# Optimization experiments

Hardware: AMD Instinct MI355X
Metric: run time of the kernel (lower is better)

Reference implementation:

```python
import jax, jax.numpy as jnp
import numpy as np

B = 32768
Z_DIM = 64
X_DIM = 256
HIDDEN = 512
T = 8            # num_transforms
NBINS = 8
TAIL = 25.0
MULT = 3 * NBINS - 1   # widths + heights + interior derivatives = 23
MIN_W = 1e-3
MIN_H = 1e-3
MIN_D = 1e-3


def _masks():
    # MADE degrees (nflows, random_mask=False)
    d_in = np.arange(1, Z_DIM + 1)                      # input degrees 1..D
    h = np.arange(HIDDEN) % (Z_DIM - 1) + 1             # hidden degrees
    o = np.arange(Z_DIM * MULT) // MULT + 1             # output degrees, MULT contiguous per feature
    m1 = (h[:, None] >= d_in[None, :]).astype(np.float32)   # [H, D]
    m2 = (h[:, None] >= h[None, :]).astype(np.float32)      # [H, H]
    m3 = (o[:, None] > h[None, :]).astype(np.float32)       # [D*MULT, H] strict for output layer
    return jnp.asarray(m1), jnp.asarray(m2), jnp.asarray(m3)


def _rq_spline_fwd(z, uw, uh, ud):
    """Unconstrained rational-quadratic spline with linear tails (forward).
    z: [B, D]; uw/uh: [B, D, NBINS]; ud: [B, D, NBINS-1].
    Returns (outputs [B,D], logabsdet [B,D])."""
    const = np.log(np.exp(1.0 - MIN_D) - 1.0)
    pad = jnp.full(ud.shape[:-1] + (1,), const, ud.dtype)
    ud = jnp.concatenate([pad, ud, pad], axis=-1)       # [B, D, NBINS+1]

    widths = jax.nn.softmax(uw, axis=-1)
    widths = MIN_W + (1.0 - MIN_W * NBINS) * widths
    zero = jnp.zeros(widths.shape[:-1] + (1,), widths.dtype)
    cumw = jnp.concatenate([zero, jnp.cumsum(widths, axis=-1)], axis=-1)
    cumw = -TAIL + 2.0 * TAIL * cumw
    cumw = cumw.at[..., 0].set(-TAIL).at[..., -1].set(TAIL)
    widths = cumw[..., 1:] - cumw[..., :-1]

    derivs = MIN_D + jax.nn.softplus(ud)

    heights = jax.nn.softmax(uh, axis=-1)
    heights = MIN_H + (1.0 - MIN_H * NBINS) * heights
    cumh = jnp.concatenate([zero, jnp.cumsum(heights, axis=-1)], axis=-1)
    cumh = -TAIL + 2.0 * TAIL * cumh
    cumh = cumh.at[..., 0].set(-TAIL).at[..., -1].set(TAIL)
    heights = cumh[..., 1:] - cumh[..., :-1]

    delta = heights / widths

    z_in = jnp.clip(z, -TAIL, TAIL)
    edges = cumw.at[..., -1].add(1e-6)                  # nflows searchsorted eps
    idx = jnp.sum(z_in[..., None] >= edges, axis=-1) - 1
    idx = jnp.clip(idx, 0, NBINS - 1)

    g = lambda a: jnp.take_along_axis(a, idx[..., None], axis=-1)[..., 0]
    in_cw = g(cumw); in_w = g(widths)
    in_ch = g(cumh); in_h = g(heights)
    in_dl = g(delta)
    d0 = g(derivs); d1 = g(derivs[..., 1:])

    th = (z_in - in_cw) / in_w
    th1 = th * (1.0 - th)
    num = in_h * (in_dl * th * th + d0 * th1)
    den = in_dl + (d0 + d1 - 2.0 * in_dl) * th1
    out = in_ch + num / den
    dnum = in_dl ** 2 * (d1 * th * th + 2.0 * in_dl * th1 + d0 * (1.0 - th) ** 2)
    lad = jnp.log(dnum) - 2.0 * jnp.log(den)

    inside = (z >= -TAIL) & (z <= TAIL)
    return jnp.where(inside, out, z), jnp.where(inside, lad, 0.0)


def setup_inputs() -> dict:
    key = jax.random.key(0)
    ks = jax.random.split(key, 10)
    s = 0.05  # small init scale keeps spline params in a sane regime
    return {
        "z": jax.random.normal(ks[0], (B, Z_DIM), jnp.float32),
        "x": jax.random.normal(ks[1], (B, X_DIM), jnp.float32),
        "W1": jax.random.normal(ks[2], (T, HIDDEN, Z_DIM), jnp.float32) * s,
        "b1": jax.random.normal(ks[3], (T, HIDDEN), jnp.float32) * s,
        "Wc": jax.random.normal(ks[4], (T, HIDDEN, X_DIM), jnp.float32) * s,
        "bc": jax.random.normal(ks[5], (T, HIDDEN), jnp.float32) * s,
        "W2": jax.random.normal(ks[6], (T, HIDDEN, HIDDEN), jnp.float32) * s,
        "b2": jax.random.normal(ks[7], (T, HIDDEN), jnp.float32) * s,
        "W3": jax.random.normal(ks[8], (T, Z_DIM * MULT, HIDDEN), jnp.float32) * s,
        "b3": jax.random.normal(ks[9], (T, Z_DIM * MULT), jnp.float32) * s,
    }


def reference(z, x, W1, b1, Wc, bc, W2, b2, W3, b3):
    """log q(z|x) of the composed MADE-RQ-spline flow, shape [B]."""
    m1, m2, m3 = _masks()
    inv_sqrt_h = 1.0 / np.sqrt(HIDDEN)
    cur = z
    total_lad = jnp.zeros(z.shape[0], z.dtype)
    for t in range(T):
        # MADE: masked initial layer + context layer, one masked feedforward block (linear->relu), masked output layer
        h = cur @ (W1[t] * m1).T + b1[t] + x @ Wc[t].T + bc[t]
        h = jax.nn.relu(h @ (W2[t] * m2).T + b2[t])
        p = (h @ (W3[t] * m3).T + b3[t]).reshape(-1, Z_DIM, MULT)
        uw = p[..., :NBINS] * inv_sqrt_h
        uh = p[..., NBINS:2 * NBINS] * inv_sqrt_h
        ud = p[..., 2 * NBINS:]
        cur, lad = _rq_spline_fwd(cur, uw, uh, ud)
        total_lad = total_lad + lad.sum(axis=-1)
    log_base = -0.5 * jnp.sum(cur ** 2, axis=-1) - 0.5 * Z_DIM * np.log(2.0 * np.pi)
    return log_base + total_lad
```

## Files before the change

### kernel.cpp

```cpp
#include <hip/hip_runtime.h>
#include <cstdint>
#include <cstddef>

#define B_ROWS 32768
#define ZD 64
#define XD 256
#define HID 512
#define T_STEPS 8
#define MULT 23
#define MPAD 24
#define NOUT 1472
#define NPAD 1536
#define K1 320
#define PSTRIDE 200

typedef float f32x4 __attribute__((ext_vector_type(4)));
typedef short s16x8 __attribute__((ext_vector_type(8)));

__device__ __forceinline__ unsigned short f2bf(float f) {
  unsigned int u = __float_as_uint(f);
  u = (u + 0x7FFFu + ((u >> 16) & 1u)) >> 16;
  return (unsigned short)u;
}
__device__ __forceinline__ float bf2f(unsigned short s) {
  return __uint_as_float(((unsigned int)s) << 16);
}

__device__ __forceinline__ int permP(int n) {
  return (n < 72) ? (n / 9) + 63 * (n % 9)
                  : ((n - 72) >> 3) + 8 + 63 * ((n - 72) & 7);
}
__device__ __forceinline__ int degP(int n) {
  return (n < 72) ? (n / 9) + 1 : ((n - 72) >> 3) + 9;
}


__global__ void prep_w1cat(const float* __restrict__ W1, const float* __restrict__ Wc,
                           unsigned short* __restrict__ o) {
  int i = blockIdx.x * 256 + threadIdx.x;
  if (i >= T_STEPS * HID * K1) return;
  int t = i / (HID * K1);
  int r = i - t * (HID * K1);
  int n = r / K1;
  int k = r - n * K1;
  int on = permP(n);
  float v;
  if (k < ZD) {
    v = ((on % 63) >= k) ? W1[((size_t)t * HID + on) * ZD + k] : 0.0f;
  } else {
    v = Wc[((size_t)t * HID + on) * XD + (k - ZD)];
  }
  o[i] = f2bf(v);
}

__global__ void prep_w2(const float* __restrict__ W2, unsigned short* __restrict__ o) {
  int i = blockIdx.x * 256 + threadIdx.x;
  if (i >= T_STEPS * HID * HID) return;
  int t = i / (HID * HID);
  int r = i - t * (HID * HID);
  int n = r / HID;
  int k = r - n * HID;
  float v = 0.0f;
  if (degP(n) >= degP(k))
    v = W2[((size_t)t * HID + permP(n)) * HID + permP(k)];
  o[i] = f2bf(v);
}

__global__ void prep_w3(const float* __restrict__ W3, unsigned short* __restrict__ o) {
  int i = blockIdx.x * 256 + threadIdx.x;
  if (i >= T_STEPS * NPAD * HID) return;
  int t = i / (NPAD * HID);
  int r = i - t * (NPAD * HID);
  int n = r / HID;
  int k = r - n * HID;
  int d = n / MPAD;
  int jj = n - d * MPAD;
  float v = 0.0f;
  if (jj < MULT && d >= degP(k))
    v = W3[((size_t)t * NOUT + d * MULT + jj) * HID + permP(k)];
  o[i] = f2bf(v);
}

__global__ void prep_bias(const float* __restrict__ b1, const float* __restrict__ bc,
                          const float* __restrict__ b2, const float* __restrict__ b3,
                          float* __restrict__ ob1, float* __restrict__ ob2,
                          float* __restrict__ ob3) {
  int i = blockIdx.x * 256 + threadIdx.x;
  if (i < T_STEPS * HID) {
    int t = i / HID, n = i - t * HID;
    int on = permP(n);
    ob1[i] = b1[(size_t)t * HID + on] + bc[(size_t)t * HID + on];
  } else if (i < 2 * T_STEPS * HID) {
    int j = i - T_STEPS * HID;
    int t = j / HID, n = j - t * HID;
    ob2[j] = b2[(size_t)t * HID + permP(n)];
  } else {
    int j = i - 2 * T_STEPS * HID;
    if (j < T_STEPS * NPAD) {
      int t = j / NPAD;
      int n = j - t * NPAD;
      int d = n / MPAD;
      int jj = n - d * MPAD;
      ob3[j] = (jj < MULT) ? b3[(size_t)t * NOUT + d * MULT + jj] : 0.0f;
    }
  }
}

__global__ void prep_x(const float* __restrict__ x, unsigned short* __restrict__ A1) {
  int i = blockIdx.x * 256 + threadIdx.x;
  if (i >= B_ROWS * XD) return;
  int b = i >> 8;
  int j = i & 255;
  A1[(size_t)b * K1 + ZD + j] = f2bf(x[i]);
}

__global__ void prep_init(const float* __restrict__ z, unsigned short* __restrict__ A1,
                          float* __restrict__ curf, float* __restrict__ lad) {
  int i = blockIdx.x * 256 + threadIdx.x;
  if (i >= B_ROWS * ZD) return;
  int b = i >> 6;
  int d = i & 63;
  float zv = z[i];
  A1[(size_t)b * K1 + d] = f2bf(zv);
  curf[i] = zv;
  if (d == 0) lad[b] = 0.0f;
}


#define ASYNC16(gp, lp) __builtin_amdgcn_global_load_lds( \
    (__attribute__((address_space(1))) unsigned int*)(gp), \
    (__attribute__((address_space(3))) unsigned int*)(lp), 16, 0, 0)


__global__ __launch_bounds__(256, 2) void gemm_bias(
    const unsigned short* __restrict__ A,
    const unsigned short* __restrict__ Bw,
    const float* __restrict__ bias,
    unsigned short* __restrict__ C,
    int M, int N, int K, int relu, int tri)
{
  __shared__ alignas(16) unsigned short lA[2 * 128 * 32];
  __shared__ alignas(16) unsigned short lB[2 * 128 * 32];

  const int tid  = threadIdx.x;
  const int lane = tid & 63;
  const int wave = tid >> 6;

  const int lin = blockIdx.y * 4 + blockIdx.x;
  const int xcd = lin & 7;
  const int loc = lin >> 3;
  const int m0 = (xcd * 32 + (loc >> 2)) * 128;
  const int n0 = (loc & 3) * 128;
  const int Keff = tri ? min(K, 192 + n0) : K;

  const int wm = (wave >> 1) * 64;
  const int wn = (wave & 1) * 64;

  const int f    = tid * 16;
  const int row0 = f >> 6;
  const int colb = f & 63;

  char* gA0 = (char*)A  + ((size_t)(m0 + row0) * K) * 2 + colb;
  char* gA1 = gA0 + (size_t)64 * K * 2;
  char* gB0 = (char*)Bw + ((size_t)(n0 + row0) * K) * 2 + colb;
  char* gB1 = gB0 + (size_t)64 * K * 2;

  unsigned short* lA0 = lA + wave * 512;
  unsigned short* lA1 = lA + 2048 + wave * 512;
  unsigned short* lB0 = lB + wave * 512;
  unsigned short* lB1 = lB + 2048 + wave * 512;

  f32x4 acc[4][4];
#pragma unroll
  for (int i = 0; i < 4; i++)
#pragma unroll
    for (int j = 0; j < 4; j++) acc[i][j] = (f32x4){0.f, 0.f, 0.f, 0.f};

  const int fr = lane & 15;
  const int fk = (lane >> 4) * 8;

  for (int k0 = 0; k0 < Keff; k0 += 64) {
    ASYNC16(gA0, lA0);
    ASYNC16(gA1, lA1);
    ASYNC16(gB0, lB0);
    ASYNC16(gB1, lB1);
    ASYNC16(gA0 + 64, lA0 + 4096);
    ASYNC16(gA1 + 64, lA1 + 4096);
    ASYNC16(gB0 + 64, lB0 + 4096);
    ASYNC16(gB1 + 64, lB1 + 4096);
    gA0 += 128; gA1 += 128; gB0 += 128; gB1 += 128;
    __syncthreads();

    s16x8 a0[4], b0[4], a1[4], b1[4];
#pragma unroll
    for (int i = 0; i < 4; i++) {
      a0[i] = *(const s16x8*)(lA + (wm + i * 16 + fr) * 32 + fk);
      a1[i] = *(const s16x8*)(lA + 4096 + (wm + i * 16 + fr) * 32 + fk);
    }
#pragma unroll
    for (int j = 0; j < 4; j++) {
      b0[j] = *(const s16x8*)(lB + (wn + j * 16 + fr) * 32 + fk);
      b1[j] = *(const s16x8*)(lB + 4096 + (wn + j * 16 + fr) * 32 + fk);
    }

#pragma unroll
    for (int i = 0; i < 4; i++)
#pragma unroll
      for (int j = 0; j < 4; j++)
        acc[i][j] = __builtin_amdgcn_mfma_f32_16x16x32_bf16(a0[i], b0[j], acc[i][j], 0, 0, 0);
#pragma unroll
    for (int i = 0; i < 4; i++)
#pragma unroll
      for (int j = 0; j < 4; j++)
        acc[i][j] = __builtin_amdgcn_mfma_f32_16x16x32_bf16(a1[i], b1[j], acc[i][j], 0, 0, 0);
    __syncthreads();
  }

#pragma unroll
  for (int j = 0; j < 4; j++) {
    const int col = n0 + wn + j * 16 + fr;
    const float bv = bias[col];
#pragma unroll
    for (int i = 0; i < 4; i++) {
      const int rbase = m0 + wm + i * 16 + (lane >> 4) * 4;
#pragma unroll
      for (int r = 0; r < 4; r++) {
        float v = acc[i][j][r] + bv;
        if (relu) v = fmaxf(v, 0.0f);
        C[(size_t)(rbase + r) * N + col] = f2bf(v);
      }
    }
  }
}


__device__ __forceinline__ void rq_spline(const unsigned short* __restrict__ pp,
                                          float zv, float& zn, float& lad) {
  const float TAILC = 25.0f;
  const float MIN_WC = 0.001f;
  const float MIN_DC = 0.001f;
  const float SCALE = 0.044194173824159216f;

  s16x8 vw = *(const s16x8*)(pp);
  s16x8 vh = *(const s16x8*)(pp + 8);
  s16x8 vd = *(const s16x8*)(pp + 16);

  bool inside = (zv >= -TAILC) && (zv <= TAILC);
  float z_in = fminf(fmaxf(zv, -TAILC), TAILC);

  float ew[8], eh[8], sw = 0.f, sh = 0.f;
#pragma unroll
  for (int i = 0; i < 8; i++) {
    float u = fminf(fmaxf(bf2f((unsigned short)vw[i]) * SCALE, -30.f), 30.f);
    ew[i] = __expf(u); sw += ew[i];
  }
#pragma unroll
  for (int i = 0; i < 8; i++) {
    float u = fminf(fmaxf(bf2f((unsigned short)vh[i]) * SCALE, -30.f), 30.f);
    eh[i] = __expf(u); sh += eh[i];
  }
  float iw = (1.0f - 8.0f * MIN_WC) / sw;
  float ih = (1.0f - 8.0f * MIN_WC) / sh;

  float cumw[9], cumh[9];
  cumw[0] = -TAILC; cumh[0] = -TAILC;
  float cw = 0.f, ch = 0.f;
#pragma unroll
  for (int i = 0; i < 8; i++) {
    cw += MIN_WC + ew[i] * iw;
    ch += MIN_WC + eh[i] * ih;
    cumw[i + 1] = fmaf(2.0f * TAILC, cw, -TAILC);
    cumh[i + 1] = fmaf(2.0f * TAILC, ch, -TAILC);
  }
  cumw[8] = TAILC; cumh[8] = TAILC;

  int idx = 0;
#pragma unroll
  for (int i = 1; i < 8; i++) idx += (z_in >= cumw[i]) ? 1 : 0;

  float in_cw = 0.f, cw1 = 1.f, in_ch = 0.f, ch1 = 1.f, u0 = 0.f, u1 = 0.f;
#pragma unroll
  for (int i = 0; i < 8; i++) {
    if (i == idx) {
      in_cw = cumw[i]; cw1 = cumw[i + 1];
      in_ch = cumh[i]; ch1 = cumh[i + 1];
      u0 = (i > 0) ? bf2f((unsigned short)vd[i - 1]) : 0.0f;
      u1 = (i < 7) ? bf2f((unsigned short)vd[i]) : 0.0f;
    }
  }
  float dd0 = (idx == 0) ? 1.0f
            : MIN_DC + fmaxf(u0, 0.f) + __logf(1.0f + __expf(-fabsf(u0)));
  float dd1 = (idx == 7) ? 1.0f
            : MIN_DC + fmaxf(u1, 0.f) + __logf(1.0f + __expf(-fabsf(u1)));
  float in_w = cw1 - in_cw;
  float in_h = ch1 - in_ch;

  float delta = in_h / in_w;
  float th  = (z_in - in_cw) / in_w;
  float th1 = th * (1.0f - th);
  float th2 = th * th;
  float num = in_h * (delta * th2 + dd0 * th1);
  float den = delta + (dd0 + dd1 - 2.0f * delta) * th1;
  float outz = in_ch + num / den;
  float omt = 1.0f - th;
  float dnum = delta * delta * (dd1 * th2 + 2.0f * delta * th1 + dd0 * omt * omt);
  float l = __logf(dnum) - 2.0f * __logf(den);

  zn  = inside ? outz : zv;
  lad = inside ? l : 0.0f;
}


__global__ __launch_bounds__(256, 2) void gemm3_spline(
    const unsigned short* __restrict__ A,
    const unsigned short* __restrict__ Bw,
    const float* __restrict__ bias,
    float* __restrict__ curf,
    unsigned short* __restrict__ A1,
    float* __restrict__ lad_acc)
{
  __shared__ alignas(16) union {
    struct { unsigned short A[2 * 128 * 32]; unsigned short B[2 * 192 * 32]; } g;
    unsigned short p[128 * PSTRIDE];
  } sm;

  const int tid  = threadIdx.x;
  const int lane = tid & 63;
  const int wave = tid >> 6;

  const int lin = blockIdx.y * 8 + blockIdx.x;
  const int xcd = lin & 7;
  const int loc = lin >> 3;
  const int m0 = (xcd * 32 + (loc >> 3)) * 128;
  const int bn = loc & 7;
  const int n0 = bn * 192;
  const int Keff = 64 * (bn + 1);

  const int wm = (wave >> 1) * 64;
  const int wn = (wave & 1) * 96;
  const int fr = lane & 15;
  const int fk = (lane >> 4) * 8;

  const int srow = tid & 127;
  const int sb = m0 + srow;
  const int dl0 = (tid >> 7) * 4;
  const int d0 = bn * 8 + dl0;
  float4 cz = *(const float4*)(curf + (size_t)sb * ZD + d0);
  float bv[6];
#pragma unroll
  for (int j = 0; j < 6; j++) bv[j] = bias[n0 + wn + j * 16 + fr];

  const int f    = tid * 16;
  const int row0 = f >> 6;
  const int colb = f & 63;
  const int K = HID;

  char* gA0 = (char*)A  + ((size_t)(m0 + row0) * K) * 2 + colb;
  char* gA1 = gA0 + (size_t)64 * K * 2;
  char* gB0 = (char*)Bw + ((size_t)(n0 + row0) * K) * 2 + colb;
  char* gB1 = gB0 + (size_t)64 * K * 2;
  char* gB2 = gB1 + (size_t)64 * K * 2;

  unsigned short* lA0 = sm.g.A + wave * 512;
  unsigned short* lA1 = sm.g.A + 2048 + wave * 512;
  unsigned short* lB0 = sm.g.B + wave * 512;
  unsigned short* lB1 = sm.g.B + 2048 + wave * 512;
  unsigned short* lB2 = sm.g.B + 4096 + wave * 512;

  f32x4 acc[4][6];
#pragma unroll
  for (int i = 0; i < 4; i++)
#pragma unroll
    for (int j = 0; j < 6; j++) acc[i][j] = (f32x4){0.f, 0.f, 0.f, 0.f};

  for (int k0 = 0; k0 < Keff; k0 += 64) {
    ASYNC16(gA0, lA0);
    ASYNC16(gA1, lA1);
    ASYNC16(gB0, lB0);
    ASYNC16(gB1, lB1);
    ASYNC16(gB2, lB2);
    ASYNC16(gA0 + 64, lA0 + 4096);
    ASYNC16(gA1 + 64, lA1 + 4096);
    ASYNC16(gB0 + 64, lB0 + 6144);
    ASYNC16(gB1 + 64, lB1 + 6144);
    ASYNC16(gB2 + 64, lB2 + 6144);
    gA0 += 128; gA1 += 128; gB0 += 128; gB1 += 128; gB2 += 128;
    __syncthreads();

    s16x8 a0[4], a1[4], b0[6], b1[6];
#pragma unroll
    for (int i = 0; i < 4; i++) {
      a0[i] = *(const s16x8*)(sm.g.A + (wm + i * 16 + fr) * 32 + fk);
      a1[i] = *(const s16x8*)(sm.g.A + 4096 + (wm + i * 16 + fr) * 32 + fk);
    }
#pragma unroll
    for (int j = 0; j < 6; j++) {
      b0[j] = *(const s16x8*)(sm.g.B + (wn + j * 16 + fr) * 32 + fk);
      b1[j] = *(const s16x8*)(sm.g.B + 6144 + (wn + j * 16 + fr) * 32 + fk);
    }

#pragma unroll
    for (int i = 0; i < 4; i++)
#pragma unroll
      for (int j = 0; j < 6; j++)
        acc[i][j] = __builtin_amdgcn_mfma_f32_16x16x32_bf16(a0[i], b0[j], acc[i][j], 0, 0, 0);
#pragma unroll
    for (int i = 0; i < 4; i++)
#pragma unroll
      for (int j = 0; j < 6; j++)
        acc[i][j] = __builtin_amdgcn_mfma_f32_16x16x32_bf16(a1[i], b1[j], acc[i][j], 0, 0, 0);
    __syncthreads();
  }

#pragma unroll
  for (int j = 0; j < 6; j++) {
    const int col = wn + j * 16 + fr;
#pragma unroll
    for (int i = 0; i < 4; i++) {
      const int rbase = wm + i * 16 + (lane >> 4) * 4;
#pragma unroll
      for (int r = 0; r < 4; r++)
        sm.p[(rbase + r) * PSTRIDE + col] = f2bf(acc[i][j][r] + bv[j]);
    }
  }
  __syncthreads();

  const unsigned short* pp = sm.p + srow * PSTRIDE + dl0 * MPAD;
  float zn0, zn1, zn2, zn3, l0, l1, l2, l3;
  rq_spline(pp,            cz.x, zn0, l0);
  rq_spline(pp + MPAD,     cz.y, zn1, l1);
  rq_spline(pp + 2 * MPAD, cz.z, zn2, l2);
  rq_spline(pp + 3 * MPAD, cz.w, zn3, l3);

  *(float4*)(curf + (size_t)sb * ZD + d0) = make_float4(zn0, zn1, zn2, zn3);
  union { unsigned int u[2]; unsigned short s[4]; } pk;
  pk.s[0] = f2bf(zn0); pk.s[1] = f2bf(zn1); pk.s[2] = f2bf(zn2); pk.s[3] = f2bf(zn3);
  *(uint2*)(A1 + (size_t)sb * K1 + d0) = make_uint2(pk.u[0], pk.u[1]);

  atomicAdd(&lad_acc[sb], l0 + l1 + l2 + l3);
}


__global__ void finalize(const float* __restrict__ curf, const float* __restrict__ lad,
                         float* __restrict__ out) {
  int i = blockIdx.x * 256 + threadIdx.x;
  int b = i >> 6;
  int d = i & 63;
  float c = curf[i];
  float q = c * c;
#pragma unroll
  for (int off = 32; off > 0; off >>= 1) q += __shfl_xor(q, off, 64);
  if (d == 0) out[b] = lad[b] - 0.5f * q - 58.81206612509905f;
}


extern "C" void kernel_launch(void* const* d_in, const int* in_sizes, int n_in,
                              void* d_out, int out_size, void* d_ws, size_t ws_size,
                              hipStream_t stream)
{
  const float* z  = (const float*)d_in[0];
  const float* x  = (const float*)d_in[1];
  const float* W1 = (const float*)d_in[2];
  const float* b1 = (const float*)d_in[3];
  const float* Wc = (const float*)d_in[4];
  const float* bc = (const float*)d_in[5];
  const float* W2 = (const float*)d_in[6];
  const float* b2 = (const float*)d_in[7];
  const float* W3 = (const float*)d_in[8];
  const float* b3 = (const float*)d_in[9];
  float* out = (float*)d_out;
  char* ws = (char*)d_ws;

  size_t oA1 = 0;
  size_t oH1 = oA1 + (size_t)B_ROWS * K1 * 2;
  size_t oH2 = oH1 + (size_t)B_ROWS * HID * 2;
  size_t oCU = oH2 + (size_t)B_ROWS * HID * 2;
  size_t oLA = oCU + (size_t)B_ROWS * ZD * 4;
  size_t oW1 = oLA + (size_t)B_ROWS * 4;
  size_t oW2 = oW1 + (size_t)T_STEPS * HID * K1 * 2;
  size_t oW3 = oW2 + (size_t)T_STEPS * HID * HID * 2;
  size_t oB1 = oW3 + (size_t)T_STEPS * NPAD * HID * 2;
  size_t oB2 = oB1 + (size_t)T_STEPS * HID * 4;
  size_t oB3 = oB2 + (size_t)T_STEPS * HID * 4;

  unsigned short* A1  = (unsigned short*)(ws + oA1);
  unsigned short* h1  = (unsigned short*)(ws + oH1);
  unsigned short* h2  = (unsigned short*)(ws + oH2);
  float* curf = (float*)(ws + oCU);
  float* lad  = (float*)(ws + oLA);
  unsigned short* w1c = (unsigned short*)(ws + oW1);
  unsigned short* w2c = (unsigned short*)(ws + oW2);
  unsigned short* w3c = (unsigned short*)(ws + oW3);
  float* b1c = (float*)(ws + oB1);
  float* b2p = (float*)(ws + oB2);
  float* b3c = (float*)(ws + oB3);

  prep_w1cat<<<T_STEPS * HID * K1 / 256, 256, 0, stream>>>(W1, Wc, w1c);
  prep_w2<<<T_STEPS * HID * HID / 256, 256, 0, stream>>>(W2, w2c);
  prep_w3<<<T_STEPS * NPAD * HID / 256, 256, 0, stream>>>(W3, w3c);
  prep_bias<<<T_STEPS * (2 * HID + NPAD) / 256, 256, 0, stream>>>(
      b1, bc, b2, b3, b1c, b2p, b3c);
  prep_x<<<B_ROWS * XD / 256, 256, 0, stream>>>(x, A1);
  prep_init<<<B_ROWS * ZD / 256, 256, 0, stream>>>(z, A1, curf, lad);

  for (int t = 0; t < T_STEPS; ++t) {
    gemm_bias<<<dim3(4, B_ROWS / 128), 256, 0, stream>>>(
        A1, w1c + (size_t)t * HID * K1, b1c + (size_t)t * HID, h1,
        B_ROWS, HID, K1, 0, 0);
    gemm_bias<<<dim3(4, B_ROWS / 128), 256, 0, stream>>>(
        h1, w2c + (size_t)t * HID * HID, b2p + (size_t)t * HID, h2,
        B_ROWS, HID, HID, 1, 1);
    gemm3_spline<<<dim3(8, B_ROWS / 128), 256, 0, stream>>>(
        h2, w3c + (size_t)t * NPAD * HID, b3c + (size_t)t * NPAD,
        curf, A1, lad);
  }
  finalize<<<B_ROWS * ZD / 256, 256, 0, stream>>>(curf, lad, out);
}
```

Before: 989.2 us.

## Merge prep kernels, fold finalize into last spline step, use exp2/log2

Merges the six preprocessing kernels into two launches and removes the finalize kernel. The last spline step now adds the base log-density term directly into the output through atomics, and the output is initialised with the constant. The spline math uses exp2f/log2 with pre-scaled constants and drops the clamps, and the GEMM launch bounds are raised to 3 blocks per SM. This trims launch count and a pass over curf, but may add register pressure, and removing the clamps risks overflow for large logits.

New measurement: 963.3 us. 1.03x faster.

```diff
diff --git a/kernel.cpp b/kernel.cpp
--- a/kernel.cpp
+++ b/kernel.cpp
@@ -35,95 +35,92 @@
 }
 
 
-__global__ void prep_w1cat(const float* __restrict__ W1, const float* __restrict__ Wc,
-                           unsigned short* __restrict__ o) {
+__global__ void prep_weights(const float* __restrict__ W1, const float* __restrict__ Wc,
+                             const float* __restrict__ W2, const float* __restrict__ W3,
+                             const float* __restrict__ b1, const float* __restrict__ bc,
+                             const float* __restrict__ b2, const float* __restrict__ b3,
+                             unsigned short* __restrict__ w1c, unsigned short* __restrict__ w2c,
+                             unsigned short* __restrict__ w3c,
+                             float* __restrict__ ob1, float* __restrict__ ob2,
+                             float* __restrict__ ob3) {
+  const int S1 = T_STEPS * HID * K1;
+  const int S2 = S1 + T_STEPS * HID * HID;
+  const int S3 = S2 + T_STEPS * NPAD * HID;
+  const int S4 = S3 + T_STEPS * HID;
+  const int S5 = S4 + T_STEPS * HID;
+  const int S6 = S5 + T_STEPS * NPAD;
   int i = blockIdx.x * 256 + threadIdx.x;
-  if (i >= T_STEPS * HID * K1) return;
-  int t = i / (HID * K1);
-  int r = i - t * (HID * K1);
-  int n = r / K1;
-  int k = r - n * K1;
-  int on = permP(n);
-  float v;
-  if (k < ZD) {
-    v = ((on % 63) >= k) ? W1[((size_t)t * HID + on) * ZD + k] : 0.0f;
-  } else {
-    v = Wc[((size_t)t * HID + on) * XD + (k - ZD)];
-  }
-  o[i] = f2bf(v);
-}
-
-__global__ void prep_w2(const float* __restrict__ W2, unsigned short* __restrict__ o) {
-  int i = blockIdx.x * 256 + threadIdx.x;
-  if (i >= T_STEPS * HID * HID) return;
-  int t = i / (HID * HID);
-  int r = i - t * (HID * HID);
-  int n = r / HID;
-  int k = r - n * HID;
-  float v = 0.0f;
-  if (degP(n) >= degP(k))
-    v = W2[((size_t)t * HID + permP(n)) * HID + permP(k)];
-  o[i] = f2bf(v);
-}
-
-__global__ void prep_w3(const float* __restrict__ W3, unsigned short* __restrict__ o) {
-  int i = blockIdx.x * 256 + threadIdx.x;
-  if (i >= T_STEPS * NPAD * HID) return;
-  int t = i / (NPAD * HID);
-  int r = i - t * (NPAD * HID);
-  int n = r / HID;
-  int k = r - n * HID;
-  int d = n / MPAD;
-  int jj = n - d * MPAD;
-  float v = 0.0f;
-  if (jj < MULT && d >= degP(k))
-    v = W3[((size_t)t * NOUT + d * MULT + jj) * HID + permP(k)];
-  o[i] = f2bf(v);
-}
-
-__global__ void prep_bias(const float* __restrict__ b1, const float* __restrict__ bc,
-                          const float* __restrict__ b2, const float* __restrict__ b3,
-                          float* __restrict__ ob1, float* __restrict__ ob2,
-                          float* __restrict__ ob3) {
-  int i = blockIdx.x * 256 + threadIdx.x;
-  if (i < T_STEPS * HID) {
-    int t = i / HID, n = i - t * HID;
+  if (i < S1) {
+    int t = i / (HID * K1);
+    int r = i - t * (HID * K1);
+    int n = r / K1;
+    int k = r - n * K1;
     int on = permP(n);
-    ob1[i] = b1[(size_t)t * HID + on] + bc[(size_t)t * HID + on];
-  } else if (i < 2 * T_STEPS * HID) {
-    int j = i - T_STEPS * HID;
+    float v;
+    if (k < ZD) v = ((on % 63) >= k) ? W1[((size_t)t * HID + on) * ZD + k] : 0.0f;
+    else        v = Wc[((size_t)t * HID + on) * XD + (k - ZD)];
+    w1c[i] = f2bf(v);
+  } else if (i < S2) {
+    int j = i - S1;
+    int t = j / (HID * HID);
+    int r = j - t * (HID * HID);
+    int n = r / HID;
+    int k = r - n * HID;
+    float v = 0.0f;
+    if (degP(n) >= degP(k))
+      v = W2[((size_t)t * HID + permP(n)) * HID + permP(k)];
+    w2c[j] = f2bf(v);
+  } else if (i < S3) {
+    int j = i - S2;
+    int t = j / (NPAD * HID);
+    int r = j - t * (NPAD * HID);
+    int n = r / HID;
+    int k = r - n * HID;
+    int d = n / MPAD;
+    int jj = n - d * MPAD;
+    float v = 0.0f;
+    if (jj < MULT && d >= degP(k))
+      v = W3[((size_t)t * NOUT + d * MULT + jj) * HID + permP(k)];
+    w3c[j] = f2bf(v);
+  } else if (i < S4) {
+    int j = i - S3;
+    int t = j / HID, n = j - t * HID;
+    int on = permP(n);
+    ob1[j] = b1[(size_t)t * HID + on] + bc[(size_t)t * HID + on];
+  } else if (i < S5) {
+    int j = i - S4;
     int t = j / HID, n = j - t * HID;
     ob2[j] = b2[(size_t)t * HID + permP(n)];
+  } else if (i < S6) {
+    int j = i - S5;
+    int t = j / NPAD;
+    int n = j - t * NPAD;
+    int d = n / MPAD;
+    int jj = n - d * MPAD;
+    ob3[j] = (jj < MULT) ? b3[(size_t)t * NOUT + d * MULT + jj] : 0.0f;
+  }
+}
+
+__global__ void prep_data(const float* __restrict__ x, const float* __restrict__ z,
+                          unsigned short* __restrict__ A1,
+                          float* __restrict__ curf, float* __restrict__ out) {
+  const int SX = B_ROWS * XD;
+  int i = blockIdx.x * 256 + threadIdx.x;
+  if (i < SX) {
+    int b = i >> 8;
+    int j = i & 255;
+    A1[(size_t)b * K1 + ZD + j] = f2bf(x[i]);
   } else {
-    int j = i - 2 * T_STEPS * HID;
-    if (j < T_STEPS * NPAD) {
-      int t = j / NPAD;
-      int n = j - t * NPAD;
-      int d = n / MPAD;
-      int jj = n - d * MPAD;
-      ob3[j] = (jj < MULT) ? b3[(size_t)t * NOUT + d * MULT + jj] : 0.0f;
-    }
-  }
-}
-
-__global__ void prep_x(const float* __restrict__ x, unsigned short* __restrict__ A1) {
-  int i = blockIdx.x * 256 + threadIdx.x;
-  if (i >= B_ROWS * XD) return;
-  int b = i >> 8;
-  int j = i & 255;
-  A1[(size_t)b * K1 + ZD + j] = f2bf(x[i]);
-}
-
-__global__ void prep_init(const float* __restrict__ z, unsigned short* __restrict__ A1,
-                          float* __restrict__ curf, float* __restrict__ lad) {
-  int i = blockIdx.x * 256 + threadIdx.x;
-  if (i >= B_ROWS * ZD) return;
-  int b = i >> 6;
-  int d = i & 63;
-  float zv = z[i];
-  A1[(size_t)b * K1 + d] = f2bf(zv);
-  curf[i] = zv;
-  if (d == 0) lad[b] = 0.0f;
+    int j = i - SX;
+    if (j < B_ROWS * ZD) {
+      int b = j >> 6;
+      int d = j & 63;
+      float zv = z[j];
+      A1[(size_t)b * K1 + d] = f2bf(zv);
+      curf[j] = zv;
+      if (d == 0) out[b] = -58.81206612509905f;
+    }
+  }
 }
 
 
@@ -132,7 +129,7 @@
     (__attribute__((address_space(3))) unsigned int*)(lp), 16, 0, 0)
 
 
-__global__ __launch_bounds__(256, 2) void gemm_bias(
+__global__ __launch_bounds__(256, 3) void gemm_bias(
     const unsigned short* __restrict__ A,
     const unsigned short* __restrict__ Bw,
     const float* __restrict__ bias,
@@ -239,7 +236,8 @@
   const float TAILC = 25.0f;
   const float MIN_WC = 0.001f;
   const float MIN_DC = 0.001f;
-  const float SCALE = 0.044194173824159216f;
+  const float SCALE2 = 0.06376007120095582f;
+  const float LN2 = 0.6931471805599453f;
 
   s16x8 vw = *(const s16x8*)(pp);
   s16x8 vh = *(const s16x8*)(pp + 8);
@@ -251,13 +249,11 @@
   float ew[8], eh[8], sw = 0.f, sh = 0.f;
 #pragma unroll
   for (int i = 0; i < 8; i++) {
-    float u = fminf(fmaxf(bf2f((unsigned short)vw[i]) * SCALE, -30.f), 30.f);
-    ew[i] = __expf(u); sw += ew[i];
+    ew[i] = exp2f(bf2f((unsigned short)vw[i]) * SCALE2); sw += ew[i];
   }
 #pragma unroll
   for (int i = 0; i < 8; i++) {
-    float u = fminf(fmaxf(bf2f((unsigned short)vh[i]) * SCALE, -30.f), 30.f);
-    eh[i] = __expf(u); sh += eh[i];
+    eh[i] = exp2f(bf2f((unsigned short)vh[i]) * SCALE2); sh += eh[i];
   }
   float iw = (1.0f - 8.0f * MIN_WC) / sw;
   float ih = (1.0f - 8.0f * MIN_WC) / sh;
@@ -304,7 +300,7 @@
   float outz = in_ch + num / den;
   float omt = 1.0f - th;
   float dnum = delta * delta * (dd1 * th2 + 2.0f * delta * th1 + dd0 * omt * omt);
-  float l = __logf(dnum) - 2.0f * __logf(den);
+  float l = LN2 * (__log2f(dnum) - 2.0f * __log2f(den));
 
   zn  = inside ? outz : zv;
   lad = inside ? l : 0.0f;
@@ -317,7 +313,8 @@
     const float* __restrict__ bias,
     float* __restrict__ curf,
     unsigned short* __restrict__ A1,
-    float* __restrict__ lad_acc)
+    float* __restrict__ out,
+    int last)
 {
   __shared__ alignas(16) union {
     struct { unsigned short A[2 * 128 * 32]; unsigned short B[2 * 192 * 32]; } g;
@@ -437,20 +434,10 @@
   pk.s[0] = f2bf(zn0); pk.s[1] = f2bf(zn1); pk.s[2] = f2bf(zn2); pk.s[3] = f2bf(zn3);
   *(uint2*)(A1 + (size_t)sb * K1 + d0) = make_uint2(pk.u[0], pk.u[1]);
 
-  atomicAdd(&lad_acc[sb], l0 + l1 + l2 + l3);
-}
-
-
-__global__ void finalize(const float* __restrict__ curf, const float* __restrict__ lad,
-                         float* __restrict__ out) {
-  int i = blockIdx.x * 256 + threadIdx.x;
-  int b = i >> 6;
-  int d = i & 63;
-  float c = curf[i];
-  float q = c * c;
-#pragma unroll
-  for (int off = 32; off > 0; off >>= 1) q += __shfl_xor(q, off, 64);
-  if (d == 0) out[b] = lad[b] - 0.5f * q - 58.81206612509905f;
+  float contrib = l0 + l1 + l2 + l3;
+  if (last)
+    contrib -= 0.5f * (zn0 * zn0 + zn1 * zn1 + zn2 * zn2 + zn3 * zn3);
+  atomicAdd(&out[sb], contrib);
 }
 
 
@@ -475,8 +462,7 @@
   size_t oH1 = oA1 + (size_t)B_ROWS * K1 * 2;
   size_t oH2 = oH1 + (size_t)B_ROWS * HID * 2;
   size_t oCU = oH2 + (size_t)B_ROWS * HID * 2;
-  size_t oLA = oCU + (size_t)B_ROWS * ZD * 4;
-  size_t oW1 = oLA + (size_t)B_ROWS * 4;
+  size_t oW1 = oCU + (size_t)B_ROWS * ZD * 4;
   size_t oW2 = oW1 + (size_t)T_STEPS * HID * K1 * 2;
   size_t oW3 = oW2 + (size_t)T_STEPS * HID * HID * 2;
   size_t oB1 = oW3 + (size_t)T_STEPS * NPAD * HID * 2;
@@ -487,7 +473,6 @@
   unsigned short* h1  = (unsigned short*)(ws + oH1);
   unsigned short* h2  = (unsigned short*)(ws + oH2);
   float* curf = (float*)(ws + oCU);
-  float* lad  = (float*)(ws + oLA);
   unsigned short* w1c = (unsigned short*)(ws + oW1);
   unsigned short* w2c = (unsigned short*)(ws + oW2);
   unsigned short* w3c = (unsigned short*)(ws + oW3);
@@ -495,13 +480,11 @@
   float* b2p = (float*)(ws + oB2);
   float* b3c = (float*)(ws + oB3);
 
-  prep_w1cat<<<T_STEPS * HID * K1 / 256, 256, 0, stream>>>(W1, Wc, w1c);
-  prep_w2<<<T_STEPS * HID * HID / 256, 256, 0, stream>>>(W2, w2c);
-  prep_w3<<<T_STEPS * NPAD * HID / 256, 256, 0, stream>>>(W3, w3c);
-  prep_bias<<<T_STEPS * (2 * HID + NPAD) / 256, 256, 0, stream>>>(
-      b1, bc, b2, b3, b1c, b2p, b3c);
-  prep_x<<<B_ROWS * XD / 256, 256, 0, stream>>>(x, A1);
-  prep_init<<<B_ROWS * ZD / 256, 256, 0, stream>>>(z, A1, curf, lad);
+  const int prepw_total = T_STEPS * (HID * K1 + HID * HID + NPAD * HID + 2 * HID + NPAD);
+  prep_weights<<<(prepw_total + 255) / 256, 256, 0, stream>>>(
+      W1, Wc, W2, W3, b1, bc, b2, b3, w1c, w2c, w3c, b1c, b2p, b3c);
+  const int prepd_total = B_ROWS * (XD + ZD);
+  prep_data<<<(prepd_total + 255) / 256, 256, 0, stream>>>(x, z, A1, curf, out);
 
   for (int t = 0; t < T_STEPS; ++t) {
     gemm_bias<<<dim3(4, B_ROWS / 128), 256, 0, stream>>>(
@@ -512,7 +495,6 @@
         B_ROWS, HID, HID, 1, 1);
     gemm3_spline<<<dim3(8, B_ROWS / 128), 256, 0, stream>>>(
         h2, w3c + (size_t)t * NPAD * HID, b3c + (size_t)t * NPAD,
-        curf, A1, lad);
-  }
-  finalize<<<B_ROWS * ZD / 256, 256, 0, stream>>>(curf, lad, out);
-}
+        curf, A1, out, (t == T_STEPS - 1) ? 1 : 0);
+  }
+}
```
